# Kernel tuning notes

Measured on AMD Instinct MI355X. Metric: run time of the kernel, lower is better.

## Reference

```python
import jax, jax.numpy as jnp
import numpy as np
from jax.scipy.special import logsumexp

EPS = 1e-4  # self.epsilon in the original module


def _pairwise_sqdist(a, b):
    # a: [B,n,d], b: [B,m,d] -> [B,n,m]; same math as get_distance (sum_d a^2+b^2-2ab)
    return (jnp.sum(a * a, axis=-1)[:, :, None]
            + jnp.sum(b * b, axis=-1)[:, None, :]
            - 2.0 * jnp.einsum('bnd,bmd->bnm', a, b))


def setup_inputs() -> dict:
    key = jax.random.key(0)
    kx, ky, ka, kb = jax.random.split(key, 4)
    b, t, n, m, d = 4, 16, 2048, 2048, 64
    return {
        'x': jax.random.normal(kx, (b, t, n, d), dtype=jnp.float32),
        'y': jax.random.normal(ky, (b, t, m, d), dtype=jnp.float32),
        'loga': jax.random.normal(ka, (b, t, n), dtype=jnp.float32),
        'logb': jax.random.normal(kb, (b, t, m), dtype=jnp.float32),
    }


def reference(x, y, loga, logb):
    b, t, n, d = x.shape
    m = y.shape[2]
    # time-major for scan
    xt = jnp.moveaxis(x, 1, 0)      # [t,b,n,d]
    yt = jnp.moveaxis(y, 1, 0)      # [t,b,m,d]
    lat = jnp.moveaxis(loga, 1, 0)  # [t,b,n]
    lbt = jnp.moveaxis(logb, 1, 0)  # [t,b,m]

    def step(carry, inp):
        f_prev, g_prev = carry
        x_new, y_new, x_prev, y_prev, la_prev, lb_prev, la_new = inp
        D = _pairwise_sqdist(x_new, y_prev)  # [b,n,m]
        f_new = -EPS * logsumexp((-D + g_prev[:, None, :]) / EPS + lb_prev[:, None, :], axis=2)
        D2 = _pairwise_sqdist(y_new, x_prev)  # [b,m,n]
        g_new = -EPS * logsumexp((-D2 + f_prev[:, None, :]) / EPS + la_prev[:, None, :], axis=2)
        # Original forward passes loga[:, i] for BOTH new_loga and new_logb (faithful).
        # loss is a global sum (scalar) that torch broadcasts into losses[:, i].
        loss = jnp.sum(jnp.exp(la_new) * f_new) + jnp.sum(jnp.exp(la_new) * g_new)
        return (f_new, g_new), (loss, f_new, g_new)

    f0 = jnp.zeros((b, n), x.dtype)
    g0 = jnp.zeros((b, m), x.dtype)
    xs = (xt[1:], yt[1:], xt[:-1], yt[:-1], lat[:-1], lbt[:-1], lat[1:])
    _, (loss_seq, f_seq, g_seq) = jax.lax.scan(step, (f0, g0), xs)

    losses = jnp.concatenate(
        [jnp.zeros((b, 1), x.dtype), jnp.broadcast_to(loss_seq[None, :], (b, t - 1))], axis=1)
    f = jnp.concatenate([f0[:, None, :], jnp.moveaxis(f_seq, 0, 1)], axis=1)  # [b,t,n]
    g = jnp.concatenate([g0[:, None, :], jnp.moveaxis(g_seq, 0, 1)], axis=1)  # [b,t,m]
    return losses, f, g
```

## Files before the change

### kernel.cpp

```cpp
#include <hip/hip_runtime.h>

#define Bq 4
#define Tt 16
#define Nn 2048
#define Dd 64
#define EPSc 1e-4f

typedef __attribute__((ext_vector_type(8))) short bf16x8;
typedef __attribute__((ext_vector_type(4))) float floatx4;

__device__ __forceinline__ unsigned rne_bf16(float f) {
    unsigned u = __float_as_uint(f);
    return (u + 0x7FFFu + ((u >> 16) & 1u)) >> 16;
}

__device__ __forceinline__ void load_lds16(const void* gptr, void* lptr) {
    __builtin_amdgcn_global_load_lds(
        (const __attribute__((address_space(1))) unsigned int*)gptr,
        (__attribute__((address_space(3))) unsigned int*)lptr,
        16, 0, 0);
}

__global__ void convert_kernel(const float* __restrict__ x, const float* __restrict__ y,
                               short* __restrict__ xh, short* __restrict__ xl,
                               short* __restrict__ yh, short* __restrict__ yl,
                               float* __restrict__ sqx, float* __restrict__ sqy,
                               float* __restrict__ pf0, float* __restrict__ pg0,
                               float* __restrict__ out_f, float* __restrict__ out_g,
                               float* __restrict__ loss_ws)
{
    const int tid = threadIdx.x;
    const int l = tid & 63;
    const int row = blockIdx.x * 32 + (tid >> 6) * 8 + (l >> 3);
    const int q = l & 7;
    const size_t dst = (size_t)row * 64 + (size_t)((q ^ (row & 7)) << 3);

    const float4* px = reinterpret_cast<const float4*>(x + (size_t)row * 64 + q * 8);
    float4 u0 = px[0], u1 = px[1];
    float fx[8] = {u0.x, u0.y, u0.z, u0.w, u1.x, u1.y, u1.z, u1.w};
    bf16x8 hv, lv;
    float ssx = 0.f;
#pragma unroll
    for (int e = 0; e < 8; ++e) {
        unsigned hb = rne_bf16(fx[e]);
        float hf = __uint_as_float(hb << 16);
        unsigned lb = rne_bf16(fx[e] - hf);
        hv[e] = (short)hb;
        lv[e] = (short)lb;
        ssx = fmaf(fx[e], fx[e], ssx);
    }
    *reinterpret_cast<bf16x8*>(&xh[dst]) = hv;
    *reinterpret_cast<bf16x8*>(&xl[dst]) = lv;
    ssx += __shfl_xor(ssx, 1, 64);
    ssx += __shfl_xor(ssx, 2, 64);
    ssx += __shfl_xor(ssx, 4, 64);

    const float4* py = reinterpret_cast<const float4*>(y + (size_t)row * 64 + q * 8);
    float4 v0 = py[0], v1 = py[1];
    float fy[8] = {v0.x, v0.y, v0.z, v0.w, v1.x, v1.y, v1.z, v1.w};
    float ssy = 0.f;
#pragma unroll
    for (int e = 0; e < 8; ++e) {
        unsigned hb = rne_bf16(fy[e]);
        float hf = __uint_as_float(hb << 16);
        unsigned lb = rne_bf16(fy[e] - hf);
        hv[e] = (short)hb;
        lv[e] = (short)lb;
        ssy = fmaf(fy[e], fy[e], ssy);
    }
    *reinterpret_cast<bf16x8*>(&yh[dst]) = hv;
    *reinterpret_cast<bf16x8*>(&yl[dst]) = lv;
    ssy += __shfl_xor(ssy, 1, 64);
    ssy += __shfl_xor(ssy, 2, 64);
    ssy += __shfl_xor(ssy, 4, 64);

    if (q == 0) {
        sqx[row] = ssx;
        sqy[row] = ssy;
        const int t = (row >> 11) & 15, b = row >> 15, n = row & (Nn - 1);
        if (t == 0) {
            out_f[(size_t)b * Tt * Nn + n] = 0.f;
            out_g[(size_t)b * Tt * Nn + n] = 0.f;
#pragma unroll
            for (int jc = 0; jc < 16; ++jc) {
                pf0[((size_t)b * 16 + jc) * Nn + n] = -ssx;
                pg0[((size_t)b * 16 + jc) * Nn + n] = -ssy;
            }
        }
    }
    if (blockIdx.x == 0 && tid < Tt) loss_ws[tid] = 0.f;
}

__device__ __forceinline__ void finish_body(int u, int id, int tid,
                                            const float* __restrict__ pf,
                                            const float* __restrict__ pg,
                                            const float* __restrict__ sqx,
                                            const float* __restrict__ sqy,
                                            const float* __restrict__ loga,
                                            float* __restrict__ out_f,
                                            float* __restrict__ out_g,
                                            float* __restrict__ loss_ws,
                                            float* __restrict__ red4)
{
    const int r = id * 256 + tid;
    const int b = r >> 11, i = r & (Nn - 1);
    const size_t idx = ((size_t)b * Tt + u) * Nn + i;
    float mf = 1e30f, mg = 1e30f;
#pragma unroll
    for (int jc = 0; jc < 16; ++jc) {
        mf = fminf(mf, pf[((size_t)b * 16 + jc) * Nn + i]);
        mg = fminf(mg, pg[((size_t)b * 16 + jc) * Nn + i]);
    }
    const float fn = sqx[idx] + mf, gn = sqy[idx] + mg;
    out_f[idx] = fn;
    out_g[idx] = gn;
    float contrib = expf(loga[idx]) * (fn + gn);
#pragma unroll
    for (int off = 32; off > 0; off >>= 1)
        contrib += __shfl_down(contrib, off, 64);
    const int lane = tid & 63, wid = tid >> 6;
    if (lane == 0) red4[wid] = contrib;
    __syncthreads();
    if (tid == 0)
        atomicAdd(&loss_ws[u], red4[0] + red4[1] + red4[2] + red4[3]);
}

__launch_bounds__(256, 2)
__global__ void minmat_kernel(const short* __restrict__ xh, const short* __restrict__ xl,
                              const short* __restrict__ yh, const short* __restrict__ yl,
                              const float* __restrict__ loga, const float* __restrict__ logb,
                              const float* __restrict__ sqx, const float* __restrict__ sqy,
                              const float* __restrict__ pf_in, const float* __restrict__ pg_in,
                              float* __restrict__ pf_out, float* __restrict__ pg_out,
                              float* __restrict__ out_f, float* __restrict__ out_g,
                              float* __restrict__ loss_ws, int s)
{
    __shared__ __align__(16) short Ah[8192], Al[8192], Bh[8192], Bl[8192];
    __shared__ float cbuf[128];
    __shared__ float red[256];

    const int tid = threadIdx.x;
    const int flat = blockIdx.x;

    if (flat >= 2048) {
        const int id = flat - 2048;
        if (s == 1 || id >= 32) return;
        finish_body(s - 1, id, tid, pf_in, pg_in, sqx, sqy, loga,
                    out_f, out_g, loss_ws, red);
        return;
    }

    const int z = flat & 7;
    const int rr = flat >> 3;
    const int b = z & 3;
    const int which = z >> 2;
    const int i0 = (rr & 15) * 128;
    const int jt = rr >> 4;
    const int j0 = jt * 128;

    const size_t curm = ((size_t)b * Tt + s) * Nn;
    const size_t prvm = curm - Nn;

    const short* Ahs = (which ? yh : xh) + (curm + i0) * Dd;
    const short* Als = (which ? yl : xl) + (curm + i0) * Dd;
    const short* Bhs = (which ? xh : yh) + (prvm + j0) * Dd;
    const short* Bls = (which ? xl : yl) + (prvm + j0) * Dd;
    const float* pin = which ? pf_in : pg_in;
    float* pout      = which ? pg_out : pf_out;
    const float* clog = which ? loga : logb;

    const int w = tid >> 6, l = tid & 63;
    {
        const int gb = w * 4096;
#pragma unroll
        for (int it = 0; it < 4; ++it) {
            const int lo = gb + it * 1024;
            const int go = lo + l * 16;
            load_lds16((const char*)Ahs + go, (char*)Ah + lo);
            load_lds16((const char*)Als + go, (char*)Al + lo);
            load_lds16((const char*)Bhs + go, (char*)Bh + lo);
            load_lds16((const char*)Bls + go, (char*)Bl + lo);
        }
    }

    if (tid < 128) {
        const float* pp = pin + (size_t)b * 16 * Nn + j0 + tid;
        float mn = 1e30f;
#pragma unroll
        for (int jc = 0; jc < 16; ++jc) mn = fminf(mn, pp[(size_t)jc * Nn]);
        cbuf[tid] = -mn - EPSc * clog[prvm + j0 + tid];
    }
    __syncthreads();

    const int wr = w >> 1, wc = w & 1;
    const int m0 = wr * 64, n0 = wc * 64;
    const int r15 = l & 15, g = l >> 4;
    const int swq = r15 & 7;

    floatx4 acc[4][4];
#pragma unroll
    for (int m = 0; m < 4; ++m)
#pragma unroll
        for (int n = 0; n < 4; ++n)
            acc[m][n] = floatx4{0.f, 0.f, 0.f, 0.f};

#pragma unroll
    for (int kc = 0; kc < 2; ++kc) {
        const int koff = (((kc << 2) | g) ^ swq) << 3;
        bf16x8 ah[4], al[4], bh[4], bl[4];
#pragma unroll
        for (int m = 0; m < 4; ++m) {
            const int ra = (m0 + m * 16 + r15) * 64 + koff;
            ah[m] = *reinterpret_cast<const bf16x8*>(&Ah[ra]);
            al[m] = *reinterpret_cast<const bf16x8*>(&Al[ra]);
            const int rb = (n0 + m * 16 + r15) * 64 + koff;
            bh[m] = *reinterpret_cast<const bf16x8*>(&Bh[rb]);
            bl[m] = *reinterpret_cast<const bf16x8*>(&Bl[rb]);
        }
#pragma unroll
        for (int m = 0; m < 4; ++m)
#pragma unroll
            for (int n = 0; n < 4; ++n) {
                acc[m][n] = __builtin_amdgcn_mfma_f32_16x16x32_bf16(ah[m], bh[n], acc[m][n], 0, 0, 0);
                acc[m][n] = __builtin_amdgcn_mfma_f32_16x16x32_bf16(ah[m], bl[n], acc[m][n], 0, 0, 0);
                acc[m][n] = __builtin_amdgcn_mfma_f32_16x16x32_bf16(al[m], bh[n], acc[m][n], 0, 0, 0);
            }
    }

    float cv[4];
#pragma unroll
    for (int n = 0; n < 4; ++n) cv[n] = cbuf[n0 + n * 16 + r15];

    float mm[4][4];
#pragma unroll
    for (int m = 0; m < 4; ++m)
#pragma unroll
        for (int r = 0; r < 4; ++r) {
            float v = fmaf(-2.f, acc[m][0][r], cv[0]);
            v = fminf(v, fmaf(-2.f, acc[m][1][r], cv[1]));
            v = fminf(v, fmaf(-2.f, acc[m][2][r], cv[2]));
            v = fminf(v, fmaf(-2.f, acc[m][3][r], cv[3]));
            mm[m][r] = v;
        }
#pragma unroll
    for (int off = 1; off < 16; off <<= 1)
#pragma unroll
        for (int m = 0; m < 4; ++m)
#pragma unroll
            for (int r = 0; r < 4; ++r)
                mm[m][r] = fminf(mm[m][r], __shfl_xor(mm[m][r], off, 64));

    if (r15 == 0) {
#pragma unroll
        for (int m = 0; m < 4; ++m)
#pragma unroll
            for (int r = 0; r < 4; ++r)
                red[wc * 128 + wr * 64 + m * 16 + g * 4 + r] = mm[m][r];
    }
    __syncthreads();
    if (tid < 128)
        pout[((size_t)b * 16 + jt) * Nn + i0 + tid] =
            fminf(red[tid], red[128 + tid]);
}

__global__ void finish_kernel(int u,
                              const float* __restrict__ pf, const float* __restrict__ pg,
                              const float* __restrict__ sqx, const float* __restrict__ sqy,
                              const float* __restrict__ loga,
                              float* __restrict__ out_f, float* __restrict__ out_g,
                              float* __restrict__ loss_ws)
{
    __shared__ float red4[4];
    finish_body(u, blockIdx.x, threadIdx.x, pf, pg, sqx, sqy, loga,
                out_f, out_g, loss_ws, red4);
}

__global__ void final_kernel(float* __restrict__ out_losses, const float* __restrict__ loss_ws)
{
    const int tid = threadIdx.x;
    const int t = tid & 15;
    out_losses[tid] = (t == 0) ? 0.f : loss_ws[t];
}

extern "C" void kernel_launch(void* const* d_in, const int* in_sizes, int n_in,
                              void* d_out, int out_size, void* d_ws, size_t ws_size,
                              hipStream_t stream)
{
    const float* x    = (const float*)d_in[0];
    const float* y    = (const float*)d_in[1];
    const float* loga = (const float*)d_in[2];
    const float* logb = (const float*)d_in[3];

    float* out        = (float*)d_out;
    float* out_losses = out;
    float* out_f      = out + Bq * Tt;
    float* out_g      = out_f + (size_t)Bq * Tt * Nn;

    const size_t NROW = (size_t)Bq * Tt * Nn;
    short* xh = (short*)d_ws;
    short* xl = xh + NROW * Dd;
    short* yh = xl + NROW * Dd;
    short* yl = yh + NROW * Dd;
    float* sqx = (float*)(yl + NROW * Dd);
    float* sqy = sqx + NROW;
    float* pf0 = sqy + NROW;
    float* pg0 = pf0 + NROW;
    float* pf1 = pg0 + NROW;
    float* pg1 = pf1 + NROW;
    float* loss_ws = pg1 + NROW;

    convert_kernel<<<4096, 256, 0, stream>>>(x, y, xh, xl, yh, yl,
                                             sqx, sqy, pf0, pg0,
                                             out_f, out_g, loss_ws);

    for (int s = 1; s < Tt; ++s) {
        const float* pf_in = (s & 1) ? pf0 : pf1;
        const float* pg_in = (s & 1) ? pg0 : pg1;
        float* pf_out = (s & 1) ? pf1 : pf0;
        float* pg_out = (s & 1) ? pg1 : pg0;
        minmat_kernel<<<2304, 256, 0, stream>>>(xh, xl, yh, yl, loga, logb,
                                                sqx, sqy, pf_in, pg_in,
                                                pf_out, pg_out,
                                                out_f, out_g, loss_ws, s);
    }
    finish_kernel<<<32, 256, 0, stream>>>(15, pf1, pg1, sqx, sqy, loga,
                                          out_f, out_g, loss_ws);
    final_kernel<<<1, 64, 0, stream>>>(out_losses, loss_ws);
}
```

Measured before the change: 410.4 us.

## Loop over column tiles inside persistent blocks with double-buffered B staging

Each block now keeps its 128-row A tile in registers and walks 8 column tiles of B (1024 columns), double-buffering B into LDS with async global-to-LDS loads. This cuts the grid from 2304 to 256 blocks of 512 threads and shrinks the partial-min buffers from 16 to 2 slices. The finish step is folded into the first 32 threads of every block. The intent is to reuse A across many columns, overlap B loads with MFMA work, and reduce the partial-min traffic. The cost is that only 256 blocks may underfill the GPU's compute units, and every column tile now ends with a block-wide barrier.

```diff
diff --git a/kernel.cpp b/kernel.cpp
--- a/kernel.cpp
+++ b/kernel.cpp
@@ -19,6 +19,18 @@
         (const __attribute__((address_space(1))) unsigned int*)gptr,
         (__attribute__((address_space(3))) unsigned int*)lptr,
         16, 0, 0);
+}
+
+__device__ __forceinline__ void stage16k(const short* __restrict__ gh,
+                                         const short* __restrict__ gl,
+                                         short* lh, short* ll, int w, int l)
+{
+#pragma unroll
+    for (int it = 0; it < 2; ++it) {
+        const int id = w * 2 + it;
+        load_lds16((const char*)gh + id * 1024 + l * 16, (char*)lh + id * 1024);
+        load_lds16((const char*)gl + id * 1024 + l * 16, (char*)ll + id * 1024);
+    }
 }
 
 __global__ void convert_kernel(const float* __restrict__ x, const float* __restrict__ y,
@@ -82,50 +94,16 @@
             out_f[(size_t)b * Tt * Nn + n] = 0.f;
             out_g[(size_t)b * Tt * Nn + n] = 0.f;
 #pragma unroll
-            for (int jc = 0; jc < 16; ++jc) {
-                pf0[((size_t)b * 16 + jc) * Nn + n] = -ssx;
-                pg0[((size_t)b * 16 + jc) * Nn + n] = -ssy;
+            for (int h = 0; h < 2; ++h) {
+                pf0[((size_t)b * 2 + h) * Nn + n] = -ssx;
+                pg0[((size_t)b * 2 + h) * Nn + n] = -ssy;
             }
         }
     }
     if (blockIdx.x == 0 && tid < Tt) loss_ws[tid] = 0.f;
 }
 
-__device__ __forceinline__ void finish_body(int u, int id, int tid,
-                                            const float* __restrict__ pf,
-                                            const float* __restrict__ pg,
-                                            const float* __restrict__ sqx,
-                                            const float* __restrict__ sqy,
-                                            const float* __restrict__ loga,
-                                            float* __restrict__ out_f,
-                                            float* __restrict__ out_g,
-                                            float* __restrict__ loss_ws,
-                                            float* __restrict__ red4)
-{
-    const int r = id * 256 + tid;
-    const int b = r >> 11, i = r & (Nn - 1);
-    const size_t idx = ((size_t)b * Tt + u) * Nn + i;
-    float mf = 1e30f, mg = 1e30f;
-#pragma unroll
-    for (int jc = 0; jc < 16; ++jc) {
-        mf = fminf(mf, pf[((size_t)b * 16 + jc) * Nn + i]);
-        mg = fminf(mg, pg[((size_t)b * 16 + jc) * Nn + i]);
-    }
-    const float fn = sqx[idx] + mf, gn = sqy[idx] + mg;
-    out_f[idx] = fn;
-    out_g[idx] = gn;
-    float contrib = expf(loga[idx]) * (fn + gn);
-#pragma unroll
-    for (int off = 32; off > 0; off >>= 1)
-        contrib += __shfl_down(contrib, off, 64);
-    const int lane = tid & 63, wid = tid >> 6;
-    if (lane == 0) red4[wid] = contrib;
-    __syncthreads();
-    if (tid == 0)
-        atomicAdd(&loss_ws[u], red4[0] + red4[1] + red4[2] + red4[3]);
-}
-
-__launch_bounds__(256, 2)
+__launch_bounds__(512, 2)
 __global__ void minmat_kernel(const short* __restrict__ xh, const short* __restrict__ xl,
                               const short* __restrict__ yh, const short* __restrict__ yl,
                               const float* __restrict__ loga, const float* __restrict__ logb,
@@ -135,132 +113,156 @@
                               float* __restrict__ out_f, float* __restrict__ out_g,
                               float* __restrict__ loss_ws, int s)
 {
-    __shared__ __align__(16) short Ah[8192], Al[8192], Bh[8192], Bl[8192];
-    __shared__ float cbuf[128];
-    __shared__ float red[256];
+    __shared__ __align__(16) short Ah[8192], Al[8192];
+    __shared__ __align__(16) short Bh[2][8192], Bl[2][8192];
+    __shared__ float carr[1024];
+    __shared__ float redm[512];
 
     const int tid = threadIdx.x;
+    const int w = tid >> 6, l = tid & 63;
     const int flat = blockIdx.x;
-
-    if (flat >= 2048) {
-        const int id = flat - 2048;
-        if (s == 1 || id >= 32) return;
-        finish_body(s - 1, id, tid, pf_in, pg_in, sqx, sqy, loga,
-                    out_f, out_g, loss_ws, red);
-        return;
-    }
-
     const int z = flat & 7;
-    const int rr = flat >> 3;
-    const int b = z & 3;
-    const int which = z >> 2;
-    const int i0 = (rr & 15) * 128;
-    const int jt = rr >> 4;
-    const int j0 = jt * 128;
+    const int b = z >> 1;
+    const int which = (z & 1) ^ (s & 1);
+    const int rr0 = flat >> 3;
+    const int i0 = (rr0 & 15) * 128;
+    const int jh = rr0 >> 4;
+    const int jbase = jh * 1024;
 
     const size_t curm = ((size_t)b * Tt + s) * Nn;
     const size_t prvm = curm - Nn;
 
     const short* Ahs = (which ? yh : xh) + (curm + i0) * Dd;
     const short* Als = (which ? yl : xl) + (curm + i0) * Dd;
-    const short* Bhs = (which ? xh : yh) + (prvm + j0) * Dd;
-    const short* Bls = (which ? xl : yl) + (prvm + j0) * Dd;
+    const short* Bhs = (which ? xh : yh) + (prvm + jbase) * Dd;
+    const short* Bls = (which ? xl : yl) + (prvm + jbase) * Dd;
     const float* pin = which ? pf_in : pg_in;
     float* pout      = which ? pg_out : pf_out;
     const float* clog = which ? loga : logb;
 
-    const int w = tid >> 6, l = tid & 63;
-    {
-        const int gb = w * 4096;
-#pragma unroll
-        for (int it = 0; it < 4; ++it) {
-            const int lo = gb + it * 1024;
-            const int go = lo + l * 16;
-            load_lds16((const char*)Ahs + go, (char*)Ah + lo);
-            load_lds16((const char*)Als + go, (char*)Al + lo);
-            load_lds16((const char*)Bhs + go, (char*)Bh + lo);
-            load_lds16((const char*)Bls + go, (char*)Bl + lo);
-        }
-    }
-
-    if (tid < 128) {
-        const float* pp = pin + (size_t)b * 16 * Nn + j0 + tid;
-        float mn = 1e30f;
-#pragma unroll
-        for (int jc = 0; jc < 16; ++jc) mn = fminf(mn, pp[(size_t)jc * Nn]);
-        cbuf[tid] = -mn - EPSc * clog[prvm + j0 + tid];
+    stage16k(Ahs, Als, Ah, Al, w, l);
+    stage16k(Bhs, Bls, Bh[0], Bl[0], w, l);
+
+    if (s >= 2 && tid < 32) {
+        const int fr = flat * 32 + tid;
+        const int fb = fr >> 11, fi = fr & (Nn - 1);
+        const size_t fidx = ((size_t)fb * Tt + (s - 1)) * Nn + fi;
+        const float mf = fminf(pf_in[((size_t)fb * 2) * Nn + fi],
+                               pf_in[((size_t)fb * 2 + 1) * Nn + fi]);
+        const float mg = fminf(pg_in[((size_t)fb * 2) * Nn + fi],
+                               pg_in[((size_t)fb * 2 + 1) * Nn + fi]);
+        const float fn = sqx[fidx] + mf, gn = sqy[fidx] + mg;
+        out_f[fidx] = fn;
+        out_g[fidx] = gn;
+        float contrib = expf(loga[fidx]) * (fn + gn);
+#pragma unroll
+        for (int off = 16; off > 0; off >>= 1)
+            contrib += __shfl_down(contrib, off, 64);
+        if (tid == 0) atomicAdd(&loss_ws[s - 1], contrib);
+    }
+
+#pragma unroll
+    for (int e = 0; e < 2; ++e) {
+        const int jj = tid * 2 + e;
+        const float p0 = pin[((size_t)b * 2) * Nn + jbase + jj];
+        const float p1 = pin[((size_t)b * 2 + 1) * Nn + jbase + jj];
+        carr[jj] = -fminf(p0, p1) - EPSc * clog[prvm + jbase + jj];
     }
     __syncthreads();
 
-    const int wr = w >> 1, wc = w & 1;
-    const int m0 = wr * 64, n0 = wc * 64;
+    const int wr = w >> 2, wc = w & 3;
+    const int m0 = wr * 64, n0 = wc * 32;
     const int r15 = l & 15, g = l >> 4;
     const int swq = r15 & 7;
 
-    floatx4 acc[4][4];
-#pragma unroll
-    for (int m = 0; m < 4; ++m)
-#pragma unroll
-        for (int n = 0; n < 4; ++n)
-            acc[m][n] = floatx4{0.f, 0.f, 0.f, 0.f};
-
+    bf16x8 ahreg[2][4], alreg[2][4];
 #pragma unroll
     for (int kc = 0; kc < 2; ++kc) {
         const int koff = (((kc << 2) | g) ^ swq) << 3;
-        bf16x8 ah[4], al[4], bh[4], bl[4];
 #pragma unroll
         for (int m = 0; m < 4; ++m) {
             const int ra = (m0 + m * 16 + r15) * 64 + koff;
-            ah[m] = *reinterpret_cast<const bf16x8*>(&Ah[ra]);
-            al[m] = *reinterpret_cast<const bf16x8*>(&Al[ra]);
-            const int rb = (n0 + m * 16 + r15) * 64 + koff;
-            bh[m] = *reinterpret_cast<const bf16x8*>(&Bh[rb]);
-            bl[m] = *reinterpret_cast<const bf16x8*>(&Bl[rb]);
+            ahreg[kc][m] = *reinterpret_cast<const bf16x8*>(&Ah[ra]);
+            alreg[kc][m] = *reinterpret_cast<const bf16x8*>(&Al[ra]);
         }
+    }
+
+    float mm[4][4];
+#pragma unroll
+    for (int m = 0; m < 4; ++m)
+#pragma unroll
+        for (int r2 = 0; r2 < 4; ++r2) mm[m][r2] = 1e30f;
+
+    for (int t = 0; t < 8; ++t) {
+        const int p = t & 1;
+        if (t < 7)
+            stage16k(Bhs + (size_t)(t + 1) * 8192, Bls + (size_t)(t + 1) * 8192,
+                     Bh[p ^ 1], Bl[p ^ 1], w, l);
+
+        bf16x8 bhr[2][2], blr[2][2];
+#pragma unroll
+        for (int kc = 0; kc < 2; ++kc) {
+            const int koff = (((kc << 2) | g) ^ swq) << 3;
+#pragma unroll
+            for (int nn = 0; nn < 2; ++nn) {
+                const int rb = (n0 + nn * 16 + r15) * 64 + koff;
+                bhr[kc][nn] = *reinterpret_cast<const bf16x8*>(&Bh[p][rb]);
+                blr[kc][nn] = *reinterpret_cast<const bf16x8*>(&Bl[p][rb]);
+            }
+        }
+
+        floatx4 acc[4][2];
 #pragma unroll
         for (int m = 0; m < 4; ++m)
 #pragma unroll
-            for (int n = 0; n < 4; ++n) {
-                acc[m][n] = __builtin_amdgcn_mfma_f32_16x16x32_bf16(ah[m], bh[n], acc[m][n], 0, 0, 0);
-                acc[m][n] = __builtin_amdgcn_mfma_f32_16x16x32_bf16(ah[m], bl[n], acc[m][n], 0, 0, 0);
-                acc[m][n] = __builtin_amdgcn_mfma_f32_16x16x32_bf16(al[m], bh[n], acc[m][n], 0, 0, 0);
+            for (int nn = 0; nn < 2; ++nn)
+                acc[m][nn] = floatx4{0.f, 0.f, 0.f, 0.f};
+
+#pragma unroll
+        for (int kc = 0; kc < 2; ++kc)
+#pragma unroll
+            for (int m = 0; m < 4; ++m)
+#pragma unroll
+                for (int nn = 0; nn < 2; ++nn) {
+                    acc[m][nn] = __builtin_amdgcn_mfma_f32_16x16x32_bf16(ahreg[kc][m], bhr[kc][nn], acc[m][nn], 0, 0, 0);
+                    acc[m][nn] = __builtin_amdgcn_mfma_f32_16x16x32_bf16(ahreg[kc][m], blr[kc][nn], acc[m][nn], 0, 0, 0);
+                    acc[m][nn] = __builtin_amdgcn_mfma_f32_16x16x32_bf16(alreg[kc][m], bhr[kc][nn], acc[m][nn], 0, 0, 0);
+                }
+
+        const float cv0 = carr[t * 128 + n0 + r15];
+        const float cv1 = carr[t * 128 + n0 + 16 + r15];
+#pragma unroll
+        for (int m = 0; m < 4; ++m)
+#pragma unroll
+            for (int r2 = 0; r2 < 4; ++r2) {
+                const float v = fminf(fmaf(-2.f, acc[m][0][r2], cv0),
+                                      fmaf(-2.f, acc[m][1][r2], cv1));
+                mm[m][r2] = fminf(mm[m][r2], v);
             }
-    }
-
-    float cv[4];
-#pragma unroll
-    for (int n = 0; n < 4; ++n) cv[n] = cbuf[n0 + n * 16 + r15];
-
-    float mm[4][4];
-#pragma unroll
-    for (int m = 0; m < 4; ++m)
-#pragma unroll
-        for (int r = 0; r < 4; ++r) {
-            float v = fmaf(-2.f, acc[m][0][r], cv[0]);
-            v = fminf(v, fmaf(-2.f, acc[m][1][r], cv[1]));
-            v = fminf(v, fmaf(-2.f, acc[m][2][r], cv[2]));
-            v = fminf(v, fmaf(-2.f, acc[m][3][r], cv[3]));
-            mm[m][r] = v;
-        }
+        __syncthreads();
+    }
+
 #pragma unroll
     for (int off = 1; off < 16; off <<= 1)
 #pragma unroll
         for (int m = 0; m < 4; ++m)
 #pragma unroll
-            for (int r = 0; r < 4; ++r)
-                mm[m][r] = fminf(mm[m][r], __shfl_xor(mm[m][r], off, 64));
+            for (int r2 = 0; r2 < 4; ++r2)
+                mm[m][r2] = fminf(mm[m][r2], __shfl_xor(mm[m][r2], off, 64));
 
     if (r15 == 0) {
 #pragma unroll
         for (int m = 0; m < 4; ++m)
 #pragma unroll
-            for (int r = 0; r < 4; ++r)
-                red[wc * 128 + wr * 64 + m * 16 + g * 4 + r] = mm[m][r];
+            for (int r2 = 0; r2 < 4; ++r2)
+                redm[wc * 128 + m0 + m * 16 + g * 4 + r2] = mm[m][r2];
     }
     __syncthreads();
-    if (tid < 128)
-        pout[((size_t)b * 16 + jt) * Nn + i0 + tid] =
-            fminf(red[tid], red[128 + tid]);
+    if (tid < 128) {
+        const float v = fminf(fminf(redm[tid], redm[128 + tid]),
+                              fminf(redm[256 + tid], redm[384 + tid]));
+        pout[((size_t)b * 2 + jh) * Nn + i0 + tid] = v;
+    }
 }
 
 __global__ void finish_kernel(int u,
@@ -270,9 +272,28 @@
                               float* __restrict__ out_f, float* __restrict__ out_g,
                               float* __restrict__ loss_ws)
 {
-    __shared__ float red4[4];
-    finish_body(u, blockIdx.x, threadIdx.x, pf, pg, sqx, sqy, loga,
-                out_f, out_g, loss_ws, red4);
+    __shared__ float red8[8];
+    const int tid = threadIdx.x;
+    const int r = blockIdx.x * 512 + tid;
+    const int b = r >> 11, i = r & (Nn - 1);
+    const size_t idx = ((size_t)b * Tt + u) * Nn + i;
+    const float mf = fminf(pf[((size_t)b * 2) * Nn + i], pf[((size_t)b * 2 + 1) * Nn + i]);
+    const float mg = fminf(pg[((size_t)b * 2) * Nn + i], pg[((size_t)b * 2 + 1) * Nn + i]);
+    const float fn = sqx[idx] + mf, gn = sqy[idx] + mg;
+    out_f[idx] = fn;
+    out_g[idx] = gn;
+    float contrib = expf(loga[idx]) * (fn + gn);
+#pragma unroll
+    for (int off = 32; off > 0; off >>= 1)
+        contrib += __shfl_down(contrib, off, 64);
+    if ((tid & 63) == 0) red8[tid >> 6] = contrib;
+    __syncthreads();
+    if (tid == 0) {
+        float ssum = 0.f;
+#pragma unroll
+        for (int k = 0; k < 8; ++k) ssum += red8[k];
+        atomicAdd(&loss_ws[u], ssum);
+    }
 }
 
 __global__ void final_kernel(float* __restrict__ out_losses, const float* __restrict__ loss_ws)
@@ -303,11 +324,12 @@
     short* yl = yh + NROW * Dd;
     float* sqx = (float*)(yl + NROW * Dd);
     float* sqy = sqx + NROW;
+    const size_t PM = (size_t)Bq * 2 * Nn;
     float* pf0 = sqy + NROW;
-    float* pg0 = pf0 + NROW;
-    float* pf1 = pg0 + NROW;
-    float* pg1 = pf1 + NROW;
-    float* loss_ws = pg1 + NROW;
+    float* pg0 = pf0 + PM;
+    float* pf1 = pg0 + PM;
+    float* pg1 = pf1 + PM;
+    float* loss_ws = pg1 + PM;
 
     convert_kernel<<<4096, 256, 0, stream>>>(x, y, xh, xl, yh, yl,
                                              sqx, sqy, pf0, pg0,
@@ -318,12 +340,12 @@
         const float* pg_in = (s & 1) ? pg0 : pg1;
         float* pf_out = (s & 1) ? pf1 : pf0;
         float* pg_out = (s & 1) ? pg1 : pg0;
-        minmat_kernel<<<2304, 256, 0, stream>>>(xh, xl, yh, yl, loga, logb,
-                                                sqx, sqy, pf_in, pg_in,
-                                                pf_out, pg_out,
-                                                out_f, out_g, loss_ws, s);
-    }
-    finish_kernel<<<32, 256, 0, stream>>>(15, pf1, pg1, sqx, sqy, loga,
+        minmat_kernel<<<256, 512, 0, stream>>>(xh, xl, yh, yl, loga, logb,
+                                               sqx, sqy, pf_in, pg_in,
+                                               pf_out, pg_out,
+                                               out_f, out_g, loss_ws, s);
+    }
+    finish_kernel<<<16, 512, 0, stream>>>(15, pf1, pg1, sqx, sqy, loga,
                                           out_f, out_g, loss_ws);
     final_kernel<<<1, 64, 0, stream>>>(out_losses, loss_ws);
 }
```

Measured after the change: 365.7 us. -10.9%, faster.
